# Performance work log

Measured on AMD Instinct MI355X. Metric: run time of the kernel, lower is better.

The kernel has to match this reference:

```python
import jax, jax.numpy as jnp
import numpy as np

TEMPERATURE = 0.2
IOU_THRESHOLD = 0.0  # all proposals kept (keep mask is all-True); identical math, jit-friendly
M, K = 8192, 128
N_CLASSES = 60


def setup_inputs() -> dict:
    key = jax.random.key(0)
    k1, k2, k3 = jax.random.split(key, 3)
    features = jax.random.normal(k1, (M, K), dtype=jnp.float32)
    ious = jax.random.uniform(k2, (M,), dtype=jnp.float32)  # in [0,1) >= 0.0 threshold
    labels = jax.random.randint(k3, (M,), 0, N_CLASSES, dtype=jnp.int64)
    return {"features": features, "ious": ious, "labels": labels}


def reference(features, ious, labels):
    # keep = ious >= IOU_THRESHOLD is all-True by construction; no compaction needed.
    # L2-normalize features along feature dim (F.normalize, dim=1)
    f = features / jnp.linalg.norm(features, axis=1, keepdims=True)
    # [M, M] cosine similarity / temperature
    sim = jnp.matmul(f, f.T) / TEMPERATURE
    # row-max subtraction (detached in original)
    sim = sim - jax.lax.stop_gradient(jnp.max(sim, axis=1, keepdims=True))
    m = sim.shape[0]
    logits_mask = 1.0 - jnp.eye(m, dtype=sim.dtype)  # zero diagonal
    exp_sim = jnp.exp(sim) * logits_mask
    log_prob = sim - jnp.log(jnp.clip(jnp.sum(exp_sim, axis=1, keepdims=True), 1e-5))
    label_mask = (labels[:, None] == labels[None, :]).astype(sim.dtype)
    per_label_log_prob = jnp.sum(log_prob * logits_mask * label_mask, axis=1) / jnp.sum(label_mask, axis=1)
    loss = -per_label_log_prob
    coef = jnp.ones_like(ious)  # reweight_func='none' -> trivial
    return jnp.mean(loss * coef)
```

## Files before the change

### kernel.cpp

```cpp
#include <hip/hip_runtime.h>
#include <hip/hip_bf16.h>

#define M_ROWS 8192
#define K_DIM 128
#define NCLS 60
#define NSLOT 64
#define NSIM 528
#define NSLAB 256

constexpr float SCL = 2.68579007f;
constexpr float LN2 = 0.69314718056f;

using f32x4 = __attribute__((ext_vector_type(4))) float;
using s16x8 = __attribute__((ext_vector_type(8))) short;

__device__ inline float bf2f(ushort u) {
    union { unsigned int i; float f; } v; v.i = ((unsigned int)u) << 16; return v.f;
}
__device__ inline float fexp2(float x) {
#if __has_builtin(__builtin_amdgcn_exp2f)
    return __builtin_amdgcn_exp2f(x);
#else
    return exp2f(x);
#endif
}


__global__ __launch_bounds__(256) void kprep(const float* __restrict__ feat,
                                             const int* __restrict__ labels,
                                             ushort* __restrict__ fnr,
                                             ushort* __restrict__ fnp,
                                             float* __restrict__ slabS,
                                             float* __restrict__ slabC,
                                             float* __restrict__ out) {
    __shared__ __align__(16) ushort ln[32][128];
    __shared__ float Sl[NCLS * K_DIM];
    __shared__ float Cl[NCLS];
    __shared__ int lab[32];
    const int tid = threadIdx.x, wv = tid >> 6, lane = tid & 63;
    const int rbase = blockIdx.x * 32;

    for (int i = tid; i < NCLS * K_DIM; i += 256) Sl[i] = 0.f;
    if (tid < NCLS) Cl[tid] = 0.f;
    if (tid < 32) lab[tid] = labels[rbase + tid];

#pragma unroll
    for (int it = 0; it < 8; ++it) {
        const int r = wv * 8 + it;
        const int grow = rbase + r;
        const float2 v = *(const float2*)&feat[(size_t)grow * K_DIM + lane * 2];
        float ss = v.x * v.x + v.y * v.y;
#pragma unroll
        for (int m = 1; m < 64; m <<= 1) ss += __shfl_xor(ss, m, 64);
        const float rs = rsqrtf(ss) * SCL;
        __hip_bfloat16 ha = __float2bfloat16(v.x * rs);
        __hip_bfloat16 hb = __float2bfloat16(v.y * rs);
        ushort2 o;
        o.x = *reinterpret_cast<const ushort*>(&ha);
        o.y = *reinterpret_cast<const ushort*>(&hb);
        *(ushort2*)&fnr[(size_t)grow * K_DIM + lane * 2] = o;
        *(ushort2*)&ln[r][lane * 2] = o;
    }
    __syncthreads();

#pragma unroll
    for (int gb = 0; gb < 2; ++gb) {
        const s16x8 vv = *(const s16x8*)&ln[gb * 16 + (tid & 15)][(tid >> 4) * 8];
        *(s16x8*)&fnp[(size_t)(blockIdx.x * 2 + gb) * 2048 + tid * 8] = vv;
    }
    if (blockIdx.x == 0 && tid == 0) out[0] = 0.f;

    const int rsub = tid >> 4;
    const int kc = tid & 15;
#pragma unroll
    for (int it = 0; it < 2; ++it) {
        const int r = it * 16 + rsub;
        const int lb = lab[r];
        if (kc == 0) atomicAdd(&Cl[lb], 1.f);
        const s16x8 q = *(const s16x8*)&ln[r][kc * 8];
        float* dst = &Sl[lb * K_DIM + kc * 8];
#pragma unroll
        for (int j = 0; j < 8; ++j) atomicAdd(&dst[j], bf2f((ushort)q[j]));
    }
    __syncthreads();
    float* oS = slabS + (size_t)blockIdx.x * (NCLS * K_DIM);
    for (int i = tid; i < NCLS * K_DIM; i += 256) oS[i] = Sl[i];
    if (tid < NCLS) slabC[blockIdx.x * 64 + tid] = Cl[tid];
}

__global__ __launch_bounds__(512) void kmain(const ushort* __restrict__ fnp,
                                             const float* __restrict__ slabS,
                                             const float* __restrict__ slabC,
                                             float* __restrict__ denomP,
                                             float* __restrict__ S,
                                             float* __restrict__ cntC) {
    __shared__ __align__(16) ushort ldsB[8 * 2048];
    __shared__ float colbuf[8][128];
    const int tid = threadIdx.x;
    const int lane = tid & 63;
    const int lrow = lane & 15;
    const int g = lane >> 4;
    const int wv = tid >> 6;

    const int bid = blockIdx.x;
    const int p = bid >> 1;
    const int h = bid & 1;
    int I = (int)((65.0f - sqrtf(4225.0f - 8.0f * (float)p)) * 0.5f);
    while ((I + 1) * 32 - ((I + 1) * I) / 2 <= p) ++I;
    while (I * 32 - (I * (I - 1)) / 2 > p) --I;
    const int J = I + (p - (I * 32 - (I * (I - 1)) / 2));
    const bool offd = (J != I);
    const int rbase = I * 256 + wv * 32;

    {
        const ushort* gbase = fnp + (size_t)(J * 16 + h * 8) * 2048;
#pragma unroll
        for (int it = 0; it < 4; ++it) {
            const int chunk = it * 512 + wv * 64;
            const ushort* src = gbase + (size_t)(chunk + lane) * 8;
            ushort* dst = &ldsB[(size_t)chunk * 8];
            __builtin_amdgcn_global_load_lds((const __attribute__((address_space(1))) void*)src,
                                             (__attribute__((address_space(3))) void*)dst, 16, 0, 0);
        }
    }

    s16x8 af[2][4];
#pragma unroll
    for (int m = 0; m < 2; ++m)
#pragma unroll
        for (int kk = 0; kk < 4; ++kk)
            af[m][kk] = *(const s16x8*)&fnp[(size_t)((rbase >> 4) + m) * 2048 + kk * 512 + lane * 8];

    __syncthreads();

    float pd[2][4] = {};

#pragma unroll
    for (int t = 0; t < 2; ++t) {
        f32x4 acc[2][4] = {};
#pragma unroll
        for (int kk = 0; kk < 4; ++kk) {
            s16x8 bfr[4];
#pragma unroll
            for (int n = 0; n < 4; ++n)
                bfr[n] = *(const s16x8*)&ldsB[(size_t)(t * 4 + n) * 2048 + kk * 512 + lane * 8];
#pragma unroll
            for (int m = 0; m < 2; ++m)
#pragma unroll
                for (int n = 0; n < 4; ++n)
                    acc[m][n] = __builtin_amdgcn_mfma_f32_16x16x32_bf16(af[m][kk], bfr[n], acc[m][n], 0, 0, 0);
        }
        float pcn[4] = {0.f, 0.f, 0.f, 0.f};
#pragma unroll
        for (int m = 0; m < 2; ++m)
#pragma unroll
            for (int n = 0; n < 4; ++n)
#pragma unroll
                for (int r = 0; r < 4; ++r) {
                    const float e = fexp2(acc[m][n][r]);
                    pd[m][r] += e;
                    pcn[n] += e;
                }
        if (offd) {
#pragma unroll
            for (int n = 0; n < 4; ++n) {
                float v = pcn[n];
                v += __shfl_xor(v, 16);
                v += __shfl_xor(v, 32);
                if (lane < 16) colbuf[wv][t * 64 + n * 16 + lrow] = v;
            }
        }
    }

#pragma unroll
    for (int m = 0; m < 2; ++m)
#pragma unroll
        for (int r = 0; r < 4; ++r) {
            float v = pd[m][r];
#pragma unroll
            for (int msk = 1; msk < 16; msk <<= 1) v += __shfl_xor(v, msk, 16);
            if (lrow == 0)
                denomP[(size_t)(2 * J + h) * M_ROWS + rbase + m * 16 + g * 4 + r] = v;
        }

    if (offd) {
        __syncthreads();
        if (tid < 128) {
            const float cv0 = colbuf[0][tid] + colbuf[1][tid] + colbuf[2][tid] + colbuf[3][tid];
            const float cv1 = colbuf[4][tid] + colbuf[5][tid] + colbuf[6][tid] + colbuf[7][tid];
            const size_t cpos = (size_t)J * 256 + h * 128 + tid;
            denomP[(size_t)(2 * I) * M_ROWS + cpos] = cv0;
            denomP[(size_t)(2 * I + 1) * M_ROWS + cpos] = cv1;
        }
    }

    if (bid < 31 && tid < 256) {
        const int i = bid * 256 + tid;
        if (i < NCLS * K_DIM) {
            float s = 0.f;
#pragma unroll 8
            for (int b = 0; b < NSLAB; ++b) s += slabS[(size_t)b * (NCLS * K_DIM) + i];
            S[i] = s;
        } else if (i < NCLS * K_DIM + NCLS) {
            const int c = i - NCLS * K_DIM;
            float s = 0.f;
#pragma unroll 8
            for (int b = 0; b < NSLAB; ++b) s += slabC[b * 64 + c];
            cntC[c] = s;
        }
    }
}

__global__ __launch_bounds__(1024) void kfin(const ushort* __restrict__ fn,
                                             const int* __restrict__ labels,
                                             const float* __restrict__ denomP,
                                             const float* __restrict__ S,
                                             const float* __restrict__ cntC,
                                             float* __restrict__ out) {
    const int tid = threadIdx.x;
    const int wv = tid >> 6, lane = tid & 63;
    const int row = blockIdx.x * 16 + wv;
    const ushort2 qv = *(const ushort2*)&fn[(size_t)row * K_DIM + lane * 2];
    const float f0 = bf2f(qv.x), f1 = bf2f(qv.y);
    const int c = labels[row];
    const float2 sv = *(const float2*)&S[c * K_DIM + lane * 2];
    float dot = f0 * sv.x + f1 * sv.y;
    float sii = f0 * f0 + f1 * f1;
    float dsum = denomP[(size_t)lane * M_ROWS + row];
#pragma unroll
    for (int msk = 1; msk < 64; msk <<= 1) {
        dot += __shfl_xor(dot, msk, 64);
        sii += __shfl_xor(sii, msk, 64);
        dsum += __shfl_xor(dsum, msk, 64);
    }

    __shared__ float ls[16];
    if (lane == 0) {
        const float cf = cntC[c];
        const float d = fmaxf(dsum - fexp2(sii), 1e-5f);
        const float p = (dot - sii) * LN2;
        ls[wv] = ((cf - 1.f) * __logf(d) - p) / cf;
    }
    __syncthreads();
    if (tid == 0) {
        float s = 0.f;
#pragma unroll
        for (int i = 0; i < 16; ++i) s += ls[i];
        atomicAdd(out, s * (1.0f / M_ROWS));
    }
}

extern "C" void kernel_launch(void* const* d_in, const int* in_sizes, int n_in,
                              void* d_out, int out_size, void* d_ws, size_t ws_size,
                              hipStream_t stream) {
    (void)in_sizes; (void)n_in; (void)out_size; (void)ws_size;
    const float* feat = (const float*)d_in[0];
    const int* labels = (const int*)d_in[2];
    float* out = (float*)d_out;
    char* ws = (char*)d_ws;
    ushort* fnr = (ushort*)ws;
    ushort* fnp = fnr + (size_t)M_ROWS * K_DIM;
    float* denomP = (float*)(fnp + (size_t)M_ROWS * K_DIM);
    float* S = denomP + (size_t)NSLOT * M_ROWS;
    float* cntC = S + NCLS * K_DIM;
    float* slabS = cntC + 64;
    float* slabC = slabS + (size_t)NSLAB * NCLS * K_DIM;

    kprep<<<M_ROWS / 32, 256, 0, stream>>>(feat, labels, fnr, fnp, slabS, slabC, out);
    kmain<<<NSIM * 2, 512, 0, stream>>>(fnp, slabS, slabC, denomP, S, cntC);
    kfin<<<M_ROWS / 16, 1024, 0, stream>>>(fnr, labels, denomP, S, cntC, out);
}
```

Before: 49.74 us.

## Compute per-class feature sums in main kernel by label scan instead of prep slabs

Result: slower. 71.04 us (+42.8%).

```diff
diff --git a/kernel.cpp b/kernel.cpp
--- a/kernel.cpp
+++ b/kernel.cpp
@@ -6,7 +6,6 @@
 #define NCLS 60
 #define NSLOT 64
 #define NSIM 528
-#define NSLAB 256
 
 constexpr float SCL = 2.68579007f;
 constexpr float LN2 = 0.69314718056f;
@@ -27,22 +26,12 @@
 
 
 __global__ __launch_bounds__(256) void kprep(const float* __restrict__ feat,
-                                             const int* __restrict__ labels,
                                              ushort* __restrict__ fnr,
                                              ushort* __restrict__ fnp,
-                                             float* __restrict__ slabS,
-                                             float* __restrict__ slabC,
                                              float* __restrict__ out) {
     __shared__ __align__(16) ushort ln[32][128];
-    __shared__ float Sl[NCLS * K_DIM];
-    __shared__ float Cl[NCLS];
-    __shared__ int lab[32];
     const int tid = threadIdx.x, wv = tid >> 6, lane = tid & 63;
     const int rbase = blockIdx.x * 32;
-
-    for (int i = tid; i < NCLS * K_DIM; i += 256) Sl[i] = 0.f;
-    if (tid < NCLS) Cl[tid] = 0.f;
-    if (tid < 32) lab[tid] = labels[rbase + tid];
 
 #pragma unroll
     for (int it = 0; it < 8; ++it) {
@@ -62,40 +51,24 @@
         *(ushort2*)&ln[r][lane * 2] = o;
     }
     __syncthreads();
-
 #pragma unroll
     for (int gb = 0; gb < 2; ++gb) {
         const s16x8 vv = *(const s16x8*)&ln[gb * 16 + (tid & 15)][(tid >> 4) * 8];
         *(s16x8*)&fnp[(size_t)(blockIdx.x * 2 + gb) * 2048 + tid * 8] = vv;
     }
     if (blockIdx.x == 0 && tid == 0) out[0] = 0.f;
-
-    const int rsub = tid >> 4;
-    const int kc = tid & 15;
-#pragma unroll
-    for (int it = 0; it < 2; ++it) {
-        const int r = it * 16 + rsub;
-        const int lb = lab[r];
-        if (kc == 0) atomicAdd(&Cl[lb], 1.f);
-        const s16x8 q = *(const s16x8*)&ln[r][kc * 8];
-        float* dst = &Sl[lb * K_DIM + kc * 8];
-#pragma unroll
-        for (int j = 0; j < 8; ++j) atomicAdd(&dst[j], bf2f((ushort)q[j]));
-    }
-    __syncthreads();
-    float* oS = slabS + (size_t)blockIdx.x * (NCLS * K_DIM);
-    for (int i = tid; i < NCLS * K_DIM; i += 256) oS[i] = Sl[i];
-    if (tid < NCLS) slabC[blockIdx.x * 64 + tid] = Cl[tid];
 }
 
 __global__ __launch_bounds__(512) void kmain(const ushort* __restrict__ fnp,
-                                             const float* __restrict__ slabS,
-                                             const float* __restrict__ slabC,
+                                             const ushort* __restrict__ fnr,
+                                             const int* __restrict__ labels,
                                              float* __restrict__ denomP,
                                              float* __restrict__ S,
                                              float* __restrict__ cntC) {
     __shared__ __align__(16) ushort ldsB[8 * 2048];
     __shared__ float colbuf[8][128];
+    __shared__ float Sb[8][128];
+    __shared__ float Cb[8];
     const int tid = threadIdx.x;
     const int lane = tid & 63;
     const int lrow = lane & 15;
@@ -194,18 +167,41 @@
         }
     }
 
-    if (bid < 31 && tid < 256) {
-        const int i = bid * 256 + tid;
-        if (i < NCLS * K_DIM) {
+    if (bid < NCLS) {
+        const int c = bid;
+        float a[8] = {0.f, 0.f, 0.f, 0.f, 0.f, 0.f, 0.f, 0.f};
+        float cnt = 0.f;
+#pragma unroll 4
+        for (int j = (tid >> 4); j < M_ROWS; j += 32) {
+            if (labels[j] == c) {
+                const s16x8 q = *(const s16x8*)&fnr[(size_t)j * K_DIM + lrow * 8];
+#pragma unroll
+                for (int i = 0; i < 8; ++i) a[i] += bf2f((ushort)q[i]);
+                if (lrow == 0) cnt += 1.f;
+            }
+        }
+#pragma unroll
+        for (int i = 0; i < 8; ++i) {
+            a[i] += __shfl_xor(a[i], 16);
+            a[i] += __shfl_xor(a[i], 32);
+        }
+        cnt += __shfl_xor(cnt, 16);
+        cnt += __shfl_xor(cnt, 32);
+        if (g == 0) {
+#pragma unroll
+            for (int i = 0; i < 8; ++i) Sb[wv][lrow * 8 + i] = a[i];
+        }
+        if (lane == 0) Cb[wv] = cnt;
+        __syncthreads();
+        if (tid < K_DIM) {
             float s = 0.f;
-#pragma unroll 8
-            for (int b = 0; b < NSLAB; ++b) s += slabS[(size_t)b * (NCLS * K_DIM) + i];
-            S[i] = s;
-        } else if (i < NCLS * K_DIM + NCLS) {
-            const int c = i - NCLS * K_DIM;
+#pragma unroll
+            for (int w = 0; w < 8; ++w) s += Sb[w][tid];
+            S[c * K_DIM + tid] = s;
+        } else if (tid == K_DIM) {
             float s = 0.f;
-#pragma unroll 8
-            for (int b = 0; b < NSLAB; ++b) s += slabC[b * 64 + c];
+#pragma unroll
+            for (int w = 0; w < 8; ++w) s += Cb[w];
             cntC[c] = s;
         }
     }
@@ -263,10 +259,8 @@
     float* denomP = (float*)(fnp + (size_t)M_ROWS * K_DIM);
     float* S = denomP + (size_t)NSLOT * M_ROWS;
     float* cntC = S + NCLS * K_DIM;
-    float* slabS = cntC + 64;
-    float* slabC = slabS + (size_t)NSLAB * NCLS * K_DIM;
-
-    kprep<<<M_ROWS / 32, 256, 0, stream>>>(feat, labels, fnr, fnp, slabS, slabC, out);
-    kmain<<<NSIM * 2, 512, 0, stream>>>(fnp, slabS, slabC, denomP, S, cntC);
+
+    kprep<<<M_ROWS / 32, 256, 0, stream>>>(feat, fnr, fnp, out);
+    kmain<<<NSIM * 2, 512, 0, stream>>>(fnp, fnr, labels, denomP, S, cntC);
     kfin<<<M_ROWS / 16, 1024, 0, stream>>>(fnr, labels, denomP, S, cntC, out);
 }
```
